# Kernel tuning notes

Measured on AMD Instinct MI355X. Metric: run time of the kernel, lower is better.

## Reference

```python
import jax, jax.numpy as jnp
import numpy as np

D_IN = 768
D_OUT = 768
NUM_HEADS = 12
HEAD_DIM = D_OUT // NUM_HEADS


def setup_inputs() -> dict:
    key = jax.random.key(0)
    ks = jax.random.split(key, 9)
    s = 1.0 / np.sqrt(D_IN)
    x = jax.random.normal(ks[0], (8, 1024, D_IN), dtype=jnp.float32)
    Wq = jax.random.uniform(ks[1], (D_IN, D_OUT), jnp.float32, -s, s)
    Wk = jax.random.uniform(ks[2], (D_IN, D_OUT), jnp.float32, -s, s)
    Wv = jax.random.uniform(ks[3], (D_IN, D_OUT), jnp.float32, -s, s)
    Wo = jax.random.uniform(ks[4], (D_OUT, D_OUT), jnp.float32, -s, s)
    bq = jax.random.uniform(ks[5], (D_OUT,), jnp.float32, -s, s)
    bk = jax.random.uniform(ks[6], (D_OUT,), jnp.float32, -s, s)
    bv = jax.random.uniform(ks[7], (D_OUT,), jnp.float32, -s, s)
    bo = jax.random.uniform(ks[8], (D_OUT,), jnp.float32, -s, s)
    return {"x": x, "Wq": Wq, "bq": bq, "Wk": Wk, "bk": bk,
            "Wv": Wv, "bv": bv, "Wo": Wo, "bo": bo}


def reference(x, Wq, bq, Wk, bk, Wv, bv, Wo, bo):
    b, n, _ = x.shape
    # projections -> (b, heads, n, head_dim)
    def split_heads(t):
        return t.reshape(b, n, NUM_HEADS, HEAD_DIM).transpose(0, 2, 1, 3)
    q = split_heads(x @ Wq + bq)
    k = split_heads(x @ Wk + bk)
    v = split_heads(x @ Wv + bv)
    scale = 1.0 / jnp.sqrt(jnp.float32(HEAD_DIM)).astype(x.dtype)
    scores = jnp.einsum('bhqd,bhkd->bhqk', q, k) * scale
    attn = jax.nn.softmax(scores, axis=-1)  # dropout p=0.0 -> identity
    ctx = jnp.einsum('bhqk,bhkd->bhqd', attn, v)
    ctx = ctx.transpose(0, 2, 1, 3).reshape(b, n, D_OUT)
    return ctx @ Wo + bo
```

## Files before the change

kernel.cpp:

```cpp
#include <hip/hip_runtime.h>
#include <math.h>

#define D_MODEL 768
#define NHEAD  12
#define HDIM   64
#define SEQ    1024
#define BATCH  8
#define MTOT   (BATCH*SEQ)
#define QKV_LD 2304

typedef _Float16 f16;
typedef __attribute__((ext_vector_type(4))) _Float16 f16x4;
typedef __attribute__((ext_vector_type(8))) _Float16 f16x8;
typedef __attribute__((ext_vector_type(4))) float f32x4;

__device__ inline void gload_lds16(const void* g, void* l) {
    __builtin_amdgcn_global_load_lds(
        (const __attribute__((address_space(1))) void*)g,
        (__attribute__((address_space(3))) void*)l, 16, 0, 0);
}

__global__ __launch_bounds__(256) void cvt_f32_f16(
    const float* __restrict__ in, f16* __restrict__ out, int n8)
{
    const int i = blockIdx.x * 256 + threadIdx.x;
    if (i < n8) {
        const float4 a = *(const float4*)(in + (size_t)i * 8);
        const float4 b = *(const float4*)(in + (size_t)i * 8 + 4);
        f16x8 v;
        v[0] = (f16)a.x; v[1] = (f16)a.y; v[2] = (f16)a.z; v[3] = (f16)a.w;
        v[4] = (f16)b.x; v[5] = (f16)b.y; v[6] = (f16)b.z; v[7] = (f16)b.w;
        *(f16x8*)(out + (size_t)i * 8) = v;
    }
}

__global__ __launch_bounds__(256) void concat_bias(
    const float* __restrict__ bq, const float* __restrict__ bk,
    const float* __restrict__ bv, float* __restrict__ bqkv)
{
    const int i = blockIdx.x * 256 + threadIdx.x;
    if (i < QKV_LD)
        bqkv[i] = (i < 768) ? bq[i] : (i < 1536) ? bk[i - 768] : bv[i - 1536];
}

__global__ __launch_bounds__(256) void transpose_cvt_all(
    const float* __restrict__ Wq, const float* __restrict__ Wk,
    const float* __restrict__ Wv, const float* __restrict__ Wo,
    f16* __restrict__ Wqkv_t, f16* __restrict__ Wo_t)
{
    const int z = blockIdx.z;
    const float* src = (z == 0) ? Wq : (z == 1) ? Wk : (z == 2) ? Wv : Wo;
    f16* dst = (z < 3) ? (Wqkv_t + (size_t)z * 768 * 768) : Wo_t;

    __shared__ f16 tile[64][72];
    const int t  = threadIdx.x;
    const int k0 = blockIdx.y * 64;
    const int n0 = blockIdx.x * 64;
    {
        const int r  = t >> 4;
        const int c4 = (t & 15) * 4;
        #pragma unroll
        for (int u = 0; u < 4; ++u) {
            const int row = r + u * 16;
            const float4 a = *(const float4*)&src[(size_t)(k0 + row) * 768 + n0 + c4];
            tile[row][c4 + 0] = (f16)a.x;
            tile[row][c4 + 1] = (f16)a.y;
            tile[row][c4 + 2] = (f16)a.z;
            tile[row][c4 + 3] = (f16)a.w;
        }
    }
    __syncthreads();
    {
        const int rn = t >> 3;
        const int ck = (t & 7) * 8;
        #pragma unroll
        for (int u = 0; u < 2; ++u) {
            const int n = rn + u * 32;
            f16x8 v;
            #pragma unroll
            for (int q = 0; q < 8; ++q) v[q] = tile[ck + q][n];
            *(f16x8*)&dst[(size_t)(n0 + n) * 768 + k0 + ck] = v;
        }
    }
}

template<typename OUT_T>
__global__ __launch_bounds__(256) void gemm_f16_tn(
    const f16* __restrict__ A, const f16* __restrict__ Bt,
    const float* __restrict__ bias, OUT_T* __restrict__ C,
    int M, int N, int K, int nb)
{
    __shared__ f16 As[128 * 32];
    __shared__ f16 Bs[128 * 32];

    const int t    = threadIdx.x;
    const int l    = t & 63;
    const int w    = t >> 6;
    const int l15  = l & 15;
    const int lg   = l >> 4;
    const int wrow = (w >> 1) * 64;
    const int wcol = (w & 1) * 64;

    const int orig = blockIdx.x;
    const int cpx  = gridDim.x >> 3;
    const int nid  = (orig & 7) * cpx + (orig >> 3);
    const int row0 = (nid / nb) * 128;
    const int col0 = (nid % nb) * 128;

    int src_row[2], src_koff[2], lds_off[2];
    #pragma unroll
    for (int i = 0; i < 2; ++i) {
        const int c = t + 256 * i;
        const int r = c >> 2;
        src_row[i]  = r;
        src_koff[i] = (((c & 3) - (r >> 1)) & 3) * 8;
        lds_off[i]  = c * 16;
    }

    int a_off[4], b_off[4];
    #pragma unroll
    for (int i = 0; i < 4; ++i) {
        const int ra = wrow + i * 16 + l15;
        a_off[i] = ra * 64 + (((lg + (ra >> 1)) & 3) * 16);
        const int rb = wcol + i * 16 + l15;
        b_off[i] = rb * 64 + (((lg + (rb >> 1)) & 3) * 16);
    }

    f32x4 acc[4][4];
    #pragma unroll
    for (int i = 0; i < 4; ++i)
        #pragma unroll
        for (int j = 0; j < 4; ++j)
            acc[i][j] = (f32x4){0.f, 0.f, 0.f, 0.f};

    const f16* Abase = A  + (size_t)row0 * K;
    const f16* Bbase = Bt + (size_t)col0 * K;

    for (int k0 = 0; k0 < K; k0 += 32) {
        #pragma unroll
        for (int i = 0; i < 2; ++i) {
            gload_lds16(Abase + (size_t)src_row[i] * K + k0 + src_koff[i],
                        (char*)As + lds_off[i]);
            gload_lds16(Bbase + (size_t)src_row[i] * K + k0 + src_koff[i],
                        (char*)Bs + lds_off[i]);
        }
        __syncthreads();

        f16x8 af[4], bf[4];
        #pragma unroll
        for (int i = 0; i < 4; ++i) {
            af[i] = *(const f16x8*)((const char*)As + a_off[i]);
            bf[i] = *(const f16x8*)((const char*)Bs + b_off[i]);
        }
        #pragma unroll
        for (int i = 0; i < 4; ++i)
            #pragma unroll
            for (int j = 0; j < 4; ++j)
                acc[i][j] = __builtin_amdgcn_mfma_f32_16x16x32_f16(
                    af[i], bf[j], acc[i][j], 0, 0, 0);
        __syncthreads();
    }

    #pragma unroll
    for (int j = 0; j < 4; ++j) {
        const int col = col0 + wcol + j * 16 + l15;
        const float bj = bias[col];
        #pragma unroll
        for (int i = 0; i < 4; ++i) {
            const int row = row0 + wrow + i * 16 + lg * 4;
            #pragma unroll
            for (int q = 0; q < 4; ++q)
                C[(size_t)(row + q) * N + col] = (OUT_T)(acc[i][j][q] + bj);
        }
    }
}

#define RESCALE_THR 10.0f

__global__ __launch_bounds__(256, 4) void attn_f16(
    const f16* __restrict__ QKV, f16* __restrict__ O)
{
    __shared__ f16 KsB[2][64 * 64];
    __shared__ f16 VtB[2][64 * 64];
    __shared__ f16 PsS[64 * 64];

    const int t   = threadIdx.x;
    const int w   = t >> 6;
    const int l   = t & 63;
    const int l15 = l & 15;
    const int lg  = l >> 4;
    const int sl  = (l15 & 7) << 4;

    const int orig = blockIdx.x;
    const int s    = (orig & 7) * 192 + (orig >> 3);
    const int bh   = s >> 4;
    const int qb   = s & 15;
    const int b  = bh / NHEAD;
    const int h  = bh % NHEAD;
    const int q0 = qb * 64;

    const size_t rowbase = (size_t)b * SEQ;
    const int qcol = h * HDIM;
    const int kcol = 768 + h * HDIM;
    const int vcol = 1536 + h * HDIM;

    const f16 hsc = (f16)(0.125f * 1.4426950408889634f);
    f16x8 qf[2];
    #pragma unroll
    for (int dc = 0; dc < 2; ++dc) {
        f16x8 v = *(const f16x8*)(QKV
            + (rowbase + q0 + w * 16 + l15) * QKV_LD
            + qcol + dc * 32 + lg * 8);
        #pragma unroll
        for (int j = 0; j < 8; ++j) v[j] *= hsc;
        qf[dc] = v;
    }

    f32x4 ctx[4];
    #pragma unroll
    for (int d2 = 0; d2 < 4; ++d2) ctx[d2] = (f32x4){0.f, 0.f, 0.f, 0.f};
    float mrun = -INFINITY;
    float lrun = 0.f;

    const int cb = w * 16;
    const f16* kptr = QKV + (rowbase + l) * QKV_LD + kcol + cb;
    const f16* vptr = QKV + (rowbase + l) * QKV_LD + vcol + cb;
    const size_t step = (size_t)64 * QKV_LD;

    f16x8 kr0 = *(const f16x8*)(kptr);
    f16x8 kr1 = *(const f16x8*)(kptr + 8);
    f16x8 vr0 = *(const f16x8*)(vptr);
    f16x8 vr1 = *(const f16x8*)(vptr + 8);

    {
        char* Kd = (char*)KsB[0];
        char* Vd = (char*)VtB[0];
        *(f16x8*)(Kd + l * 128 + ((cb * 2)      ^ ((l & 7) << 4))) = kr0;
        *(f16x8*)(Kd + l * 128 + ((cb * 2 + 16) ^ ((l & 7) << 4))) = kr1;
        #pragma unroll
        for (int j = 0; j < 8; ++j) {
            *(f16*)(Vd + (cb + j)     * 128 + ((l * 2) ^ (j << 4))) = vr0[j];
            *(f16*)(Vd + (cb + 8 + j) * 128 + ((l * 2) ^ (j << 4))) = vr1[j];
        }
    }
    kr0 = *(const f16x8*)(kptr + step);
    kr1 = *(const f16x8*)(kptr + step + 8);
    vr0 = *(const f16x8*)(vptr + step);
    vr1 = *(const f16x8*)(vptr + step + 8);
    __syncthreads();

    for (int kt = 0; kt < SEQ / 64; ++kt) {
        const int p = kt & 1;
        const char* Kp = (const char*)KsB[p];
        const char* Vp = (const char*)VtB[p];
        char* Pp = (char*)PsS;

        f32x4 sc[4];
        __builtin_amdgcn_s_setprio(1);
        #pragma unroll
        for (int kc = 0; kc < 4; ++kc) {
            const int rk = kc * 16 + l15;
            const f16x8 ka0 = *(const f16x8*)(Kp + rk * 128 + ((lg * 16)      ^ sl));
            const f16x8 ka1 = *(const f16x8*)(Kp + rk * 128 + ((64 + lg * 16) ^ sl));
            f32x4 a = (f32x4){0.f, 0.f, 0.f, 0.f};
            a = __builtin_amdgcn_mfma_f32_16x16x32_f16(ka0, qf[0], a, 0, 0, 0);
            a = __builtin_amdgcn_mfma_f32_16x16x32_f16(ka1, qf[1], a, 0, 0, 0);
            sc[kc] = a;
        }
        __builtin_amdgcn_s_setprio(0);

        {
            float tmax = fmaxf(fmaxf(sc[0][0], sc[0][1]), fmaxf(sc[0][2], sc[0][3]));
            #pragma unroll
            for (int kc = 1; kc < 4; ++kc)
                tmax = fmaxf(tmax, fmaxf(fmaxf(sc[kc][0], sc[kc][1]),
                                         fmaxf(sc[kc][2], sc[kc][3])));
            tmax = fmaxf(tmax, __shfl_xor(tmax, 16));
            tmax = fmaxf(tmax, __shfl_xor(tmax, 32));

            if (__any(tmax > mrun + RESCALE_THR)) {
                const float mnew = fmaxf(mrun, tmax);
                const float corr = exp2f(mrun - mnew);
                mrun = mnew;
                lrun *= corr;
                float cr[4];
                #pragma unroll
                for (int r = 0; r < 4; ++r)
                    cr[r] = __shfl(corr, lg * 4 + r);
                #pragma unroll
                for (int dcol = 0; dcol < 4; ++dcol)
                    #pragma unroll
                    for (int r = 0; r < 4; ++r)
                        ctx[dcol][r] *= cr[r];
            }

            float ps = 0.f;
            const int rowq = w * 16 + l15;
            #pragma unroll
            for (int kc = 0; kc < 4; ++kc) {
                f16x4 pv;
                #pragma unroll
                for (int r = 0; r < 4; ++r) {
                    const float pe = exp2f(sc[kc][r] - mrun);
                    ps += pe;
                    pv[r] = (f16)pe;
                }
                *(f16x4*)(Pp + rowq * 128 + ((kc * 32 + lg * 8) ^ sl)) = pv;
            }
            ps += __shfl_xor(ps, 16);
            ps += __shfl_xor(ps, 32);
            lrun += ps;
        }

        __builtin_amdgcn_s_setprio(1);
        #pragma unroll
        for (int kc2 = 0; kc2 < 2; ++kc2) {
            const int cbyte = (kc2 * 64 + lg * 16) ^ sl;
            const f16x8 pa = *(const f16x8*)(Pp + (w * 16 + l15) * 128 + cbyte);
            #pragma unroll
            for (int sd = 0; sd < 4; ++sd) {
                const f16x8 vb = *(const f16x8*)(Vp + (sd * 16 + l15) * 128 + cbyte);
                ctx[sd] = __builtin_amdgcn_mfma_f32_16x16x32_f16(pa, vb, ctx[sd], 0, 0, 0);
            }
        }
        __builtin_amdgcn_s_setprio(0);

        if (kt < SEQ / 64 - 1) {
            char* Kd = (char*)KsB[p ^ 1];
            char* Vd = (char*)VtB[p ^ 1];
            *(f16x8*)(Kd + l * 128 + ((cb * 2)      ^ ((l & 7) << 4))) = kr0;
            *(f16x8*)(Kd + l * 128 + ((cb * 2 + 16) ^ ((l & 7) << 4))) = kr1;
            #pragma unroll
            for (int j = 0; j < 8; ++j) {
                *(f16*)(Vd + (cb + j)     * 128 + ((l * 2) ^ (j << 4))) = vr0[j];
                *(f16*)(Vd + (cb + 8 + j) * 128 + ((l * 2) ^ (j << 4))) = vr1[j];
            }
            if (kt < SEQ / 64 - 2) {
                const f16* kp = kptr + (size_t)(kt + 2) * step;
                const f16* vp = vptr + (size_t)(kt + 2) * step;
                kr0 = *(const f16x8*)(kp);
                kr1 = *(const f16x8*)(kp + 8);
                vr0 = *(const f16x8*)(vp);
                vr1 = *(const f16x8*)(vp + 8);
            }
        }
        __syncthreads();
    }

    {
        const float inv = 1.0f / lrun;
        float iv[4];
        #pragma unroll
        for (int r = 0; r < 4; ++r)
            iv[r] = __shfl(inv, lg * 4 + r);
        #pragma unroll
        for (int r = 0; r < 4; ++r) {
            const size_t row = rowbase + q0 + w * 16 + lg * 4 + r;
            #pragma unroll
            for (int dcol = 0; dcol < 4; ++dcol)
                O[row * D_MODEL + qcol + dcol * 16 + l15] = (f16)(ctx[dcol][r] * iv[r]);
        }
    }
}

extern "C" void kernel_launch(void* const* d_in, const int* in_sizes, int n_in,
                              void* d_out, int out_size, void* d_ws, size_t ws_size,
                              hipStream_t stream) {
    const float* x  = (const float*)d_in[0];
    const float* Wq = (const float*)d_in[1];
    const float* bq = (const float*)d_in[2];
    const float* Wk = (const float*)d_in[3];
    const float* bk = (const float*)d_in[4];
    const float* Wv = (const float*)d_in[5];
    const float* bv = (const float*)d_in[6];
    const float* Wo = (const float*)d_in[7];
    const float* bo = (const float*)d_in[8];
    float* out = (float*)d_out;

    char* ws = (char*)d_ws;
    f16*   QKV     = (f16*)(ws);
    f16*   xh      = (f16*)(ws + 37748736);
    f16*   ctxh    = (f16*)(ws + 37748736 + 12582912);
    f16*   Wqkv_t  = (f16*)(ws + 37748736 + 2 * 12582912);
    f16*   Wo_t    = (f16*)(ws + 37748736 + 2 * 12582912 + 3538944);
    float* bqkv    = (float*)(ws + 37748736 + 2 * 12582912 + 3538944 + 1179648);

    hipLaunchKernelGGL(cvt_f32_f16, dim3(MTOT * D_MODEL / 8 / 256), dim3(256), 0, stream,
                       x, xh, MTOT * D_MODEL / 8);
    hipLaunchKernelGGL(concat_bias, dim3(9), dim3(256), 0, stream, bq, bk, bv, bqkv);
    hipLaunchKernelGGL(transpose_cvt_all, dim3(12, 12, 4), dim3(256), 0, stream,
                       Wq, Wk, Wv, Wo, Wqkv_t, Wo_t);

    hipLaunchKernelGGL((gemm_f16_tn<f16>), dim3((QKV_LD / 128) * (MTOT / 128)), dim3(256), 0, stream,
                       xh, Wqkv_t, bqkv, QKV, MTOT, QKV_LD, D_MODEL, QKV_LD / 128);

    hipLaunchKernelGGL(attn_f16, dim3((SEQ / 64) * BATCH * NHEAD), dim3(256), 0, stream,
                       QKV, ctxh);

    hipLaunchKernelGGL((gemm_f16_tn<float>), dim3((D_MODEL / 128) * (MTOT / 128)), dim3(256), 0, stream,
                       ctxh, Wo_t, bo, out, MTOT, D_MODEL, D_MODEL, D_MODEL / 128);
}
```

Baseline: 146.0 us.

## Switch attention to 32x32x16 MFMA with register-resident P and 128-row query tiles

Rewrites the attention kernel to use 32x32x16 MFMA instructions, with each wave handling 32 query rows, so each block covers 128 queries and half as many blocks are launched. The probability tile is no longer staged through shared memory. It is converted to packed f16 in registers and redistributed across half-waves with cross-lane shuffles to form the A operand for the PV product. V is now transposed into LDS with vectorized 4-element stores instead of scalar ones. This halves K/V reloads per query and removes the P LDS round trip, at the cost of more registers (launch bounds lowered to 3 blocks) and fewer blocks in flight.

```diff
diff --git a/kernel.cpp b/kernel.cpp
--- a/kernel.cpp
+++ b/kernel.cpp
@@ -10,9 +10,14 @@
 #define QKV_LD 2304
 
 typedef _Float16 f16;
+typedef __attribute__((ext_vector_type(2))) __fp16 fp16x2;
 typedef __attribute__((ext_vector_type(4))) _Float16 f16x4;
 typedef __attribute__((ext_vector_type(8))) _Float16 f16x8;
 typedef __attribute__((ext_vector_type(4))) float f32x4;
+typedef __attribute__((ext_vector_type(16))) float f32x16;
+
+union PFrag { unsigned u[4]; f16x8 v; };
+union PackW { fp16x2 h; unsigned u; };
 
 __device__ inline void gload_lds16(const void* g, void* l) {
     __builtin_amdgcn_global_load_lds(
@@ -176,106 +181,118 @@
 }
 
 #define RESCALE_THR 10.0f
-
-__global__ __launch_bounds__(256, 4) void attn_f16(
+#define QMAP(r, hh) (((r) & 3) + 8 * ((r) >> 2) + 4 * (hh))
+
+__global__ __launch_bounds__(256, 3) void attn_f16(
     const f16* __restrict__ QKV, f16* __restrict__ O)
 {
     __shared__ f16 KsB[2][64 * 64];
     __shared__ f16 VtB[2][64 * 64];
-    __shared__ f16 PsS[64 * 64];
 
     const int t   = threadIdx.x;
     const int w   = t >> 6;
     const int l   = t & 63;
-    const int l15 = l & 15;
-    const int lg  = l >> 4;
-    const int sl  = (l15 & 7) << 4;
+    const int l31 = l & 31;
+    const int h   = l >> 5;
+    const int sl  = (l & 7) << 4;
 
     const int orig = blockIdx.x;
-    const int s    = (orig & 7) * 192 + (orig >> 3);
-    const int bh   = s >> 4;
-    const int qb   = s & 15;
+    const int s    = (orig & 7) * 96 + (orig >> 3);
+    const int bh   = s >> 3;
+    const int qb   = s & 7;
     const int b  = bh / NHEAD;
-    const int h  = bh % NHEAD;
-    const int q0 = qb * 64;
+    const int hd = bh % NHEAD;
+    const int q0 = qb * 128;
 
     const size_t rowbase = (size_t)b * SEQ;
-    const int qcol = h * HDIM;
-    const int kcol = 768 + h * HDIM;
-    const int vcol = 1536 + h * HDIM;
+    const int qcol = hd * HDIM;
+    const int kcol = 768 + hd * HDIM;
+    const int vcol = 1536 + hd * HDIM;
 
     const f16 hsc = (f16)(0.125f * 1.4426950408889634f);
-    f16x8 qf[2];
-    #pragma unroll
-    for (int dc = 0; dc < 2; ++dc) {
+    f16x8 qf[4];
+    #pragma unroll
+    for (int dc = 0; dc < 4; ++dc) {
         f16x8 v = *(const f16x8*)(QKV
-            + (rowbase + q0 + w * 16 + l15) * QKV_LD
-            + qcol + dc * 32 + lg * 8);
+            + (rowbase + q0 + w * 32 + l31) * QKV_LD
+            + qcol + dc * 16 + h * 8);
         #pragma unroll
         for (int j = 0; j < 8; ++j) v[j] *= hsc;
         qf[dc] = v;
     }
 
-    f32x4 ctx[4];
-    #pragma unroll
-    for (int d2 = 0; d2 < 4; ++d2) ctx[d2] = (f32x4){0.f, 0.f, 0.f, 0.f};
+    f32x16 ctx[2];
+    #pragma unroll
+    for (int dt = 0; dt < 2; ++dt)
+        #pragma unroll
+        for (int r = 0; r < 16; ++r) ctx[dt][r] = 0.f;
     float mrun = -INFINITY;
     float lrun = 0.f;
 
-    const int cb = w * 16;
-    const f16* kptr = QKV + (rowbase + l) * QKV_LD + kcol + cb;
-    const f16* vptr = QKV + (rowbase + l) * QKV_LD + vcol + cb;
+    const int cb  = w * 16;
+    const int vk0 = (l & 15) * 4;
+    const int vd0 = ((l >> 4) + 4 * w) * 4;
+    const f16* kptr = QKV + (rowbase + l)   * QKV_LD + kcol + cb;
+    const f16* vptr = QKV + (rowbase + vk0) * QKV_LD + vcol + vd0;
     const size_t step = (size_t)64 * QKV_LD;
 
-    f16x8 kr0 = *(const f16x8*)(kptr);
-    f16x8 kr1 = *(const f16x8*)(kptr + 8);
-    f16x8 vr0 = *(const f16x8*)(vptr);
-    f16x8 vr1 = *(const f16x8*)(vptr + 8);
+    f16x8 kr0, kr1;
+    f16x4 vr[4];
+    kr0 = *(const f16x8*)(kptr);
+    kr1 = *(const f16x8*)(kptr + 8);
+    #pragma unroll
+    for (int i = 0; i < 4; ++i)
+        vr[i] = *(const f16x4*)(vptr + (size_t)i * QKV_LD);
 
     {
         char* Kd = (char*)KsB[0];
         char* Vd = (char*)VtB[0];
-        *(f16x8*)(Kd + l * 128 + ((cb * 2)      ^ ((l & 7) << 4))) = kr0;
-        *(f16x8*)(Kd + l * 128 + ((cb * 2 + 16) ^ ((l & 7) << 4))) = kr1;
-        #pragma unroll
-        for (int j = 0; j < 8; ++j) {
-            *(f16*)(Vd + (cb + j)     * 128 + ((l * 2) ^ (j << 4))) = vr0[j];
-            *(f16*)(Vd + (cb + 8 + j) * 128 + ((l * 2) ^ (j << 4))) = vr1[j];
+        *(f16x8*)(Kd + l * 128 + ((cb * 2)      ^ sl)) = kr0;
+        *(f16x8*)(Kd + l * 128 + ((cb * 2 + 16) ^ sl)) = kr1;
+        #pragma unroll
+        for (int di = 0; di < 4; ++di) {
+            f16x4 wt;
+            #pragma unroll
+            for (int i = 0; i < 4; ++i) wt[i] = vr[i][di];
+            *(f16x4*)(Vd + (vd0 + di) * 128
+                         + ((vk0 * 2) ^ (((vd0 + di) & 7) << 4))) = wt;
         }
     }
     kr0 = *(const f16x8*)(kptr + step);
     kr1 = *(const f16x8*)(kptr + step + 8);
-    vr0 = *(const f16x8*)(vptr + step);
-    vr1 = *(const f16x8*)(vptr + step + 8);
+    #pragma unroll
+    for (int i = 0; i < 4; ++i)
+        vr[i] = *(const f16x4*)(vptr + step + (size_t)i * QKV_LD);
     __syncthreads();
 
     for (int kt = 0; kt < SEQ / 64; ++kt) {
         const int p = kt & 1;
         const char* Kp = (const char*)KsB[p];
         const char* Vp = (const char*)VtB[p];
-        char* Pp = (char*)PsS;
-
-        f32x4 sc[4];
+
+        f32x16 sacc[2];
         __builtin_amdgcn_s_setprio(1);
         #pragma unroll
-        for (int kc = 0; kc < 4; ++kc) {
-            const int rk = kc * 16 + l15;
-            const f16x8 ka0 = *(const f16x8*)(Kp + rk * 128 + ((lg * 16)      ^ sl));
-            const f16x8 ka1 = *(const f16x8*)(Kp + rk * 128 + ((64 + lg * 16) ^ sl));
-            f32x4 a = (f32x4){0.f, 0.f, 0.f, 0.f};
-            a = __builtin_amdgcn_mfma_f32_16x16x32_f16(ka0, qf[0], a, 0, 0, 0);
-            a = __builtin_amdgcn_mfma_f32_16x16x32_f16(ka1, qf[1], a, 0, 0, 0);
-            sc[kc] = a;
+        for (int kk = 0; kk < 2; ++kk) {
+            f32x16 a;
+            #pragma unroll
+            for (int r = 0; r < 16; ++r) a[r] = 0.f;
+            #pragma unroll
+            for (int dc = 0; dc < 4; ++dc) {
+                const f16x8 ka = *(const f16x8*)(Kp + (kk * 32 + l31) * 128
+                                                    + ((dc * 32 + h * 16) ^ sl));
+                a = __builtin_amdgcn_mfma_f32_32x32x16_f16(ka, qf[dc], a, 0, 0, 0);
+            }
+            sacc[kk] = a;
         }
         __builtin_amdgcn_s_setprio(0);
 
         {
-            float tmax = fmaxf(fmaxf(sc[0][0], sc[0][1]), fmaxf(sc[0][2], sc[0][3]));
-            #pragma unroll
-            for (int kc = 1; kc < 4; ++kc)
-                tmax = fmaxf(tmax, fmaxf(fmaxf(sc[kc][0], sc[kc][1]),
-                                         fmaxf(sc[kc][2], sc[kc][3])));
-            tmax = fmaxf(tmax, __shfl_xor(tmax, 16));
+            float tmax = sacc[0][0];
+            #pragma unroll
+            for (int r = 1; r < 16; ++r) tmax = fmaxf(tmax, sacc[0][r]);
+            #pragma unroll
+            for (int r = 0; r < 16; ++r) tmax = fmaxf(tmax, sacc[1][r]);
             tmax = fmaxf(tmax, __shfl_xor(tmax, 32));
 
             if (__any(tmax > mrun + RESCALE_THR)) {
@@ -283,44 +300,62 @@
                 const float corr = exp2f(mrun - mnew);
                 mrun = mnew;
                 lrun *= corr;
-                float cr[4];
                 #pragma unroll
-                for (int r = 0; r < 4; ++r)
-                    cr[r] = __shfl(corr, lg * 4 + r);
+                for (int r = 0; r < 16; ++r) {
+                    const float cr = __shfl(corr, QMAP(r, h));
+                    ctx[0][r] *= cr;
+                    ctx[1][r] *= cr;
+                }
+            }
+
+            float ps = 0.f;
+            #pragma unroll
+            for (int kk = 0; kk < 2; ++kk)
                 #pragma unroll
-                for (int dcol = 0; dcol < 4; ++dcol)
-                    #pragma unroll
-                    for (int r = 0; r < 4; ++r)
-                        ctx[dcol][r] *= cr[r];
-            }
-
-            float ps = 0.f;
-            const int rowq = w * 16 + l15;
-            #pragma unroll
-            for (int kc = 0; kc < 4; ++kc) {
-                f16x4 pv;
-                #pragma unroll
-                for (int r = 0; r < 4; ++r) {
-                    const float pe = exp2f(sc[kc][r] - mrun);
+                for (int r = 0; r < 16; ++r) {
+                    const float pe = exp2f(sacc[kk][r] - mrun);
                     ps += pe;
-                    pv[r] = (f16)pe;
+                    sacc[kk][r] = pe;
                 }
-                *(f16x4*)(Pp + rowq * 128 + ((kc * 32 + lg * 8) ^ sl)) = pv;
-            }
-            ps += __shfl_xor(ps, 16);
             ps += __shfl_xor(ps, 32);
             lrun += ps;
         }
 
+        unsigned paw[4][4];
+        #pragma unroll
+        for (int kk = 0; kk < 2; ++kk) {
+            unsigned dw[8];
+            #pragma unroll
+            for (int i = 0; i < 8; ++i) {
+                PackW u;
+                u.h = __builtin_amdgcn_cvt_pkrtz(sacc[kk][2 * i], sacc[kk][2 * i + 1]);
+                dw[i] = u.u;
+            }
+            const unsigned t0 = (unsigned)__shfl_xor((int)(h ? dw[0] : dw[2]), 32);
+            const unsigned t1 = (unsigned)__shfl_xor((int)(h ? dw[1] : dw[3]), 32);
+            const unsigned t2 = (unsigned)__shfl_xor((int)(h ? dw[4] : dw[6]), 32);
+            const unsigned t3 = (unsigned)__shfl_xor((int)(h ? dw[5] : dw[7]), 32);
+            paw[2 * kk][0]     = h ? t0    : dw[0];
+            paw[2 * kk][1]     = h ? t1    : dw[1];
+            paw[2 * kk][2]     = h ? dw[2] : t0;
+            paw[2 * kk][3]     = h ? dw[3] : t1;
+            paw[2 * kk + 1][0] = h ? t2    : dw[4];
+            paw[2 * kk + 1][1] = h ? t3    : dw[5];
+            paw[2 * kk + 1][2] = h ? dw[6] : t2;
+            paw[2 * kk + 1][3] = h ? dw[7] : t3;
+        }
+
         __builtin_amdgcn_s_setprio(1);
         #pragma unroll
-        for (int kc2 = 0; kc2 < 2; ++kc2) {
-            const int cbyte = (kc2 * 64 + lg * 16) ^ sl;
-            const f16x8 pa = *(const f16x8*)(Pp + (w * 16 + l15) * 128 + cbyte);
-            #pragma unroll
-            for (int sd = 0; sd < 4; ++sd) {
-                const f16x8 vb = *(const f16x8*)(Vp + (sd * 16 + l15) * 128 + cbyte);
-                ctx[sd] = __builtin_amdgcn_mfma_f32_16x16x32_f16(pa, vb, ctx[sd], 0, 0, 0);
+        for (int c = 0; c < 4; ++c) {
+            PFrag pf;
+            pf.u[0] = paw[c][0]; pf.u[1] = paw[c][1];
+            pf.u[2] = paw[c][2]; pf.u[3] = paw[c][3];
+            #pragma unroll
+            for (int dt = 0; dt < 2; ++dt) {
+                const f16x8 vb = *(const f16x8*)(Vp + (dt * 32 + l31) * 128
+                                                    + ((c * 32 + h * 16) ^ sl));
+                ctx[dt] = __builtin_amdgcn_mfma_f32_32x32x16_f16(pf.v, vb, ctx[dt], 0, 0, 0);
             }
         }
         __builtin_amdgcn_s_setprio(0);
@@ -328,20 +363,24 @@
         if (kt < SEQ / 64 - 1) {
             char* Kd = (char*)KsB[p ^ 1];
             char* Vd = (char*)VtB[p ^ 1];
-            *(f16x8*)(Kd + l * 128 + ((cb * 2)      ^ ((l & 7) << 4))) = kr0;
-            *(f16x8*)(Kd + l * 128 + ((cb * 2 + 16) ^ ((l & 7) << 4))) = kr1;
-            #pragma unroll
-            for (int j = 0; j < 8; ++j) {
-                *(f16*)(Vd + (cb + j)     * 128 + ((l * 2) ^ (j << 4))) = vr0[j];
-                *(f16*)(Vd + (cb + 8 + j) * 128 + ((l * 2) ^ (j << 4))) = vr1[j];
+            *(f16x8*)(Kd + l * 128 + ((cb * 2)      ^ sl)) = kr0;
+            *(f16x8*)(Kd + l * 128 + ((cb * 2 + 16) ^ sl)) = kr1;
+            #pragma unroll
+            for (int di = 0; di < 4; ++di) {
+                f16x4 wt;
+                #pragma unroll
+                for (int i = 0; i < 4; ++i) wt[i] = vr[i][di];
+                *(f16x4*)(Vd + (vd0 + di) * 128
+                             + ((vk0 * 2) ^ (((vd0 + di) & 7) << 4))) = wt;
             }
             if (kt < SEQ / 64 - 2) {
                 const f16* kp = kptr + (size_t)(kt + 2) * step;
                 const f16* vp = vptr + (size_t)(kt + 2) * step;
                 kr0 = *(const f16x8*)(kp);
                 kr1 = *(const f16x8*)(kp + 8);
-                vr0 = *(const f16x8*)(vp);
-                vr1 = *(const f16x8*)(vp + 8);
+                #pragma unroll
+                for (int i = 0; i < 4; ++i)
+                    vr[i] = *(const f16x4*)(vp + (size_t)i * QKV_LD);
             }
         }
         __syncthreads();
@@ -349,16 +388,12 @@
 
     {
         const float inv = 1.0f / lrun;
-        float iv[4];
-        #pragma unroll
-        for (int r = 0; r < 4; ++r)
-            iv[r] = __shfl(inv, lg * 4 + r);
-        #pragma unroll
-        for (int r = 0; r < 4; ++r) {
-            const size_t row = rowbase + q0 + w * 16 + lg * 4 + r;
-            #pragma unroll
-            for (int dcol = 0; dcol < 4; ++dcol)
-                O[row * D_MODEL + qcol + dcol * 16 + l15] = (f16)(ctx[dcol][r] * iv[r]);
+        #pragma unroll
+        for (int r = 0; r < 16; ++r) {
+            const float iv = __shfl(inv, QMAP(r, h));
+            const size_t row = rowbase + q0 + w * 32 + QMAP(r, h);
+            O[row * D_MODEL + qcol + l31]      = (f16)(ctx[0][r] * iv);
+            O[row * D_MODEL + qcol + 32 + l31] = (f16)(ctx[1][r] * iv);
         }
     }
 }
@@ -394,7 +429,7 @@
     hipLaunchKernelGGL((gemm_f16_tn<f16>), dim3((QKV_LD / 128) * (MTOT / 128)), dim3(256), 0, stream,
                        xh, Wqkv_t, bqkv, QKV, MTOT, QKV_LD, D_MODEL, QKV_LD / 128);
 
-    hipLaunchKernelGGL(attn_f16, dim3((SEQ / 64) * BATCH * NHEAD), dim3(256), 0, stream,
+    hipLaunchKernelGGL(attn_f16, dim3((SEQ / 128) * BATCH * NHEAD), dim3(256), 0, stream,
                        QKV, ctxh);
 
     hipLaunchKernelGGL((gemm_f16_tn<float>), dim3((D_MODEL / 128) * (MTOT / 128)), dim3(256), 0, stream,
```

Result: faster. 139.8 us (-4.2%).
